# Kernel tuning notes

Hardware: AMD Instinct MI355X
Metric: run time of the kernel (lower is better)

## Reference

```python
import jax, jax.numpy as jnp
import numpy as np

NT, C, B, N, H, E = 32768, 128, 64, 512, 4, 524288  # total nodes, channels, graphs, nodes/graph, heads, edges
DH = C // H
EPS = 1e-5


def batchnorm(x, g, b):
    # BatchNorm1d over the node dimension (training-mode batch statistics)
    m = x.mean(axis=0)
    v = x.var(axis=0)
    return (x - m) * jax.lax.rsqrt(v + EPS) * g + b


def setup_inputs() -> dict:
    key = jax.random.key(0)
    ks = jax.random.split(key, 8)
    s = 1.0 / np.sqrt(C)
    return dict(
        x=jax.random.normal(ks[0], (NT, C), jnp.float32),
        edge_index=jax.random.randint(ks[1], (2, E), 0, NT, dtype=jnp.int32),
        Wc=jax.random.normal(ks[2], (C, C), jnp.float32) * s,
        bc=jnp.zeros((C,), jnp.float32),
        in_proj_w=jax.random.normal(ks[3], (3 * C, C), jnp.float32) * s,
        in_proj_b=jnp.zeros((3 * C,), jnp.float32),
        out_proj_w=jax.random.normal(ks[4], (C, C), jnp.float32) * s,
        out_proj_b=jnp.zeros((C,), jnp.float32),
        gn1=jnp.ones((C,), jnp.float32), bn1=jnp.zeros((C,), jnp.float32),
        gn2=jnp.ones((C,), jnp.float32), bn2=jnp.zeros((C,), jnp.float32),
        gn3=jnp.ones((C,), jnp.float32), bn3=jnp.zeros((C,), jnp.float32),
        Wm1=jax.random.normal(ks[5], (2 * C, C), jnp.float32) * s,
        bm1=jnp.zeros((2 * C,), jnp.float32),
        Wm2=jax.random.normal(ks[6], (C, 2 * C), jnp.float32) / np.sqrt(2 * C),
        bm2=jnp.zeros((C,), jnp.float32),
    )


def reference(x, edge_index, Wc, bc, in_proj_w, in_proj_b, out_proj_w, out_proj_b,
              gn1, bn1, gn2, bn2, gn3, bn3, Wm1, bm1, Wm2, bm2):
    # --- local branch: mean-aggregation message passing + linear + residual + BN ---
    src, dst = edge_index[0], edge_index[1]
    agg = jax.ops.segment_sum(x[src], dst, num_segments=NT)            # [NT, C]
    cnt = jax.ops.segment_sum(jnp.ones((E, 1), x.dtype), dst, num_segments=NT)
    agg = agg / jnp.maximum(cnt, 1.0)
    h_local = agg @ Wc.T + bc + x                                       # dropout p=0 -> no-op
    h_local = batchnorm(h_local, gn1, bn1)

    # --- global branch: to_dense_batch (equal-size graphs -> reshape) + MHA ---
    hd = x.reshape(B, N, C)
    qkv = hd @ in_proj_w.T + in_proj_b                                  # [B, N, 3C]
    q, k, v = jnp.split(qkv, 3, axis=-1)
    q = q.reshape(B, N, H, DH).transpose(0, 2, 1, 3)                    # [B, H, N, DH]
    k = k.reshape(B, N, H, DH).transpose(0, 2, 1, 3)
    v = v.reshape(B, N, H, DH).transpose(0, 2, 1, 3)
    scores = jnp.einsum('bhqd,bhkd->bhqk', q, k) / np.sqrt(DH)          # [B, H, N, N]
    attn = jax.nn.softmax(scores, axis=-1)
    o = jnp.einsum('bhqk,bhkd->bhqd', attn, v)                          # [B, H, N, DH]
    o = o.transpose(0, 2, 1, 3).reshape(B, N, C)
    h_attn = (o @ out_proj_w.T + out_proj_b).reshape(NT, C) + x
    h_attn = batchnorm(h_attn, gn2, bn2)

    # --- combine + MLP + final norm ---
    out = h_local + h_attn
    out = out + (jax.nn.relu(out @ Wm1.T + bm1) @ Wm2.T + bm2)
    return batchnorm(out, gn3, bn3)
```

## Files before the change

kernel.cpp:

```cpp
#include <hip/hip_runtime.h>
#include <cstddef>

#define NT    32768
#define CCH   128
#define BB    64
#define NNODE 512
#define NHEAD 4
#define DHEAD 32
#define EE    524288
#define EPS   1e-5f
#define MAXDEG 96

typedef unsigned short u16;
typedef unsigned int   u32;
typedef __attribute__((ext_vector_type(8))) short short8;
typedef __attribute__((ext_vector_type(4))) short short4v;
typedef __attribute__((ext_vector_type(4))) float f32x4;

__device__ __forceinline__ float b2f(u32 w) { return __uint_as_float(w << 16); }
__device__ __forceinline__ u16 f2b(float f) {
    u32 u = __float_as_uint(f);
    u += 0x7FFF + ((u >> 16) & 1);
    return (u16)(u >> 16);
}

__global__ __launch_bounds__(256) void prep_kernel(const float* __restrict__ x,
                                                   const float* __restrict__ Wc,
                                                   const float* __restrict__ Wqkv,
                                                   const float* __restrict__ Wo,
                                                   const float* __restrict__ Wm1,
                                                   const float* __restrict__ Wm2,
                                                   u16* __restrict__ xb,
                                                   u16* __restrict__ Wcb,
                                                   u16* __restrict__ Wqkvb,
                                                   u16* __restrict__ Wob,
                                                   u16* __restrict__ Wm1b,
                                                   u16* __restrict__ Wm2b,
                                                   const int* __restrict__ ei,
                                                   int* __restrict__ cursor,
                                                   int* __restrict__ bucket) {
    if (blockIdx.x >= 2120) {
        int e = (blockIdx.x - 2120) * 256 + threadIdx.x;
        int src = ei[e];
        int dst = ei[EE + e];
        int pos = atomicAdd(cursor + dst, 1);
        if (pos < MAXDEG) bucket[dst * MAXDEG + pos] = src;
        return;
    }
    int r = blockIdx.x * 256 + threadIdx.x;
    const float* src; u16* dst;
    if (r < 524288) { src = x; dst = xb; }
    else if ((r -= 524288) < 2048) { src = Wc; dst = Wcb; }
    else if ((r -= 2048) < 6144) { src = Wqkv; dst = Wqkvb; }
    else if ((r -= 6144) < 2048) { src = Wo; dst = Wob; }
    else if ((r -= 2048) < 4096) { src = Wm1; dst = Wm1b; }
    else { r -= 4096; src = Wm2; dst = Wm2b; }
    size_t base = (size_t)r * 8;
    float4 a = *(const float4*)(src + base);
    float4 b = *(const float4*)(src + base + 4);
    uint4 u;
    u.x = (u32)f2b(a.x) | ((u32)f2b(a.y) << 16);
    u.y = (u32)f2b(a.z) | ((u32)f2b(a.w) << 16);
    u.z = (u32)f2b(b.x) | ((u32)f2b(b.y) << 16);
    u.w = (u32)f2b(b.z) | ((u32)f2b(b.w) << 16);
    *(uint4*)(dst + base) = u;
}

__global__ __launch_bounds__(256) void aggregate(const int* __restrict__ bucket,
                                                 const int* __restrict__ cursor,
                                                 const u16* __restrict__ xb,
                                                 u16* __restrict__ agg) {
    int ln = threadIdx.x >> 5;
    int c4 = threadIdx.x & 31;
    int n = blockIdx.x * 8 + ln;
    __shared__ int srcs[8][MAXDEG];
    int d = min(cursor[n], MAXDEG);
    for (int j = c4; j < d; j += 32) srcs[ln][j] = bucket[n * MAXDEG + j];
    __syncthreads();
    float s0 = 0.f, s1 = 0.f, s2 = 0.f, s3 = 0.f;
    for (int j = 0; j < d; ++j) {
        uint2 w = *(const uint2*)(xb + (size_t)srcs[ln][j] * CCH + c4 * 4);
        s0 += b2f(w.x & 0xffffu);
        s1 += b2f(w.x >> 16);
        s2 += b2f(w.y & 0xffffu);
        s3 += b2f(w.y >> 16);
    }
    float inv = 1.0f / fmaxf((float)d, 1.0f);
    uint2 out;
    out.x = (u32)f2b(s0 * inv) | ((u32)f2b(s1 * inv) << 16);
    out.y = (u32)f2b(s2 * inv) | ((u32)f2b(s3 * inv) << 16);
    *(uint2*)(agg + (size_t)n * CCH + c4 * 4) = out;
}

template <bool RELU, int RESID, bool STATS>
__global__ __launch_bounds__(256) void gemm_mfma(const u16* __restrict__ A,
                                                 const u16* __restrict__ W,
                                                 const float* __restrict__ bias,
                                                 const u16* __restrict__ residb,
                                                 u16* __restrict__ outb,
                                                 float* __restrict__ sum,
                                                 float* __restrict__ sumsq,
                                                 int M, int N, int K) {
    __shared__ u16 As[128 * 32];
    __shared__ u16 Bs[128 * 32];
    __shared__ u16 Cs[4][16 * 72];
    __shared__ float csum[128];
    __shared__ float csq[128];
    int m0 = blockIdx.x * 128, n0 = blockIdx.y * 128;
    int tid = threadIdx.x;
    int lane = tid & 63, wave = tid >> 6;
    int wm = (wave & 1) * 64, wn = (wave >> 1) * 64;
    int l15 = lane & 15, l4 = lane >> 4;

    if (STATS) {
        if (tid < 128) { csum[tid] = 0.f; csq[tid] = 0.f; }
    }

    f32x4 zero = {0.f, 0.f, 0.f, 0.f};
    f32x4 acc[4][4];
#pragma unroll
    for (int i = 0; i < 4; ++i)
#pragma unroll
        for (int j = 0; j < 4; ++j) acc[i][j] = zero;

    int srow = tid >> 2;
    int scol = (tid & 3) * 8;

    int kIter = K >> 5;
    uint4 a0 = *(const uint4*)(A + (size_t)(m0 + srow) * K + scol);
    uint4 a1 = *(const uint4*)(A + (size_t)(m0 + srow + 64) * K + scol);
    uint4 b0 = *(const uint4*)(W + (size_t)(n0 + srow) * K + scol);
    uint4 b1 = *(const uint4*)(W + (size_t)(n0 + srow + 64) * K + scol);
    for (int ki = 0; ki < kIter; ++ki) {
        if (ki) __syncthreads();
        *(uint4*)&As[srow * 32 + scol] = a0;
        *(uint4*)&As[(srow + 64) * 32 + scol] = a1;
        *(uint4*)&Bs[srow * 32 + scol] = b0;
        *(uint4*)&Bs[(srow + 64) * 32 + scol] = b1;
        if (ki + 1 < kIter) {
            int k0 = (ki + 1) * 32;
            a0 = *(const uint4*)(A + (size_t)(m0 + srow) * K + k0 + scol);
            a1 = *(const uint4*)(A + (size_t)(m0 + srow + 64) * K + k0 + scol);
            b0 = *(const uint4*)(W + (size_t)(n0 + srow) * K + k0 + scol);
            b1 = *(const uint4*)(W + (size_t)(n0 + srow + 64) * K + k0 + scol);
        }
        __syncthreads();
        short8 af[4], bf[4];
#pragma unroll
        for (int t = 0; t < 4; ++t) {
            af[t] = *(const short8*)&As[(wm + t * 16 + l15) * 32 + l4 * 8];
            bf[t] = *(const short8*)&Bs[(wn + t * 16 + l15) * 32 + l4 * 8];
        }
#pragma unroll
        for (int mt = 0; mt < 4; ++mt)
#pragma unroll
            for (int nt = 0; nt < 4; ++nt)
                acc[mt][nt] = __builtin_amdgcn_mfma_f32_16x16x32_bf16(af[mt], bf[nt], acc[mt][nt], 0, 0, 0);
    }

    float ps[4] = {0.f, 0.f, 0.f, 0.f};
    float pq[4] = {0.f, 0.f, 0.f, 0.f};
    int rl = lane >> 3;
    int cg = lane & 7;
#pragma unroll
    for (int mt = 0; mt < 4; ++mt) {
#pragma unroll
        for (int nt = 0; nt < 4; ++nt) {
            int col = n0 + wn + nt * 16 + l15;
            float bs = bias[col];
#pragma unroll
            for (int r = 0; r < 4; ++r) {
                int row = m0 + wm + mt * 16 + l4 * 4 + r;
                float v = acc[mt][nt][r] + bs;
                if (RESID == 2) v += b2f(residb[(size_t)row * N + col]);
                if (RELU) v = fmaxf(v, 0.0f);
                Cs[wave][(l4 * 4 + r) * 72 + nt * 16 + l15] = f2b(v);
                if (STATS) { ps[nt] += v; pq[nt] += v * v; }
            }
        }
#pragma unroll
        for (int p = 0; p < 2; ++p) {
            int lrow = p * 8 + rl;
            uint4 wv = *(const uint4*)&Cs[wave][lrow * 72 + cg * 8];
            int grow = m0 + wm + mt * 16 + lrow;
            *(uint4*)(outb + (size_t)grow * N + n0 + wn + cg * 8) = wv;
        }
    }
    if (STATS) {
#pragma unroll
        for (int nt = 0; nt < 4; ++nt) {
            atomicAdd(&csum[wn + nt * 16 + l15], ps[nt]);
            atomicAdd(&csq[wn + nt * 16 + l15], pq[nt]);
        }
        __syncthreads();
        if (tid < 128) {
            atomicAdd(sum + n0 + tid, csum[tid]);
            atomicAdd(sumsq + n0 + tid, csq[tid]);
        }
    }
}

__global__ __launch_bounds__(256) void gemm_wc_qkv(const u16* __restrict__ aggb,
                                                   const u16* __restrict__ Wcb,
                                                   const float* __restrict__ bc,
                                                   const u16* __restrict__ xb,
                                                   u16* __restrict__ hlocb,
                                                   float* __restrict__ sum1,
                                                   float* __restrict__ sq1,
                                                   const u16* __restrict__ Wqkvb,
                                                   const float* __restrict__ bqkv,
                                                   u16* __restrict__ qkvb) {
    __shared__ u16 As[128 * 32];
    __shared__ u16 Bs[128 * 32];
    __shared__ u16 Cs[4][16 * 72];
    __shared__ float csum[128];
    __shared__ float csq[128];
    int y = blockIdx.y;
    bool wc = (y == 0);
    const u16* A = wc ? aggb : xb;
    const u16* W = wc ? Wcb : (Wqkvb + (size_t)(y - 1) * 128 * 128);
    const float* bias = wc ? bc : (bqkv + (y - 1) * 128);
    int ostride = wc ? 128 : 384;
    int ocol0 = wc ? 0 : (y - 1) * 128;
    u16* outp = wc ? hlocb : qkvb;

    int m0 = blockIdx.x * 128;
    int tid = threadIdx.x;
    int lane = tid & 63, wave = tid >> 6;
    int wm = (wave & 1) * 64, wn = (wave >> 1) * 64;
    int l15 = lane & 15, l4 = lane >> 4;

    if (wc && tid < 128) { csum[tid] = 0.f; csq[tid] = 0.f; }

    f32x4 zero = {0.f, 0.f, 0.f, 0.f};
    f32x4 acc[4][4];
#pragma unroll
    for (int i = 0; i < 4; ++i)
#pragma unroll
        for (int j = 0; j < 4; ++j) acc[i][j] = zero;

    int srow = tid >> 2;
    int scol = (tid & 3) * 8;

    uint4 a0 = *(const uint4*)(A + (size_t)(m0 + srow) * 128 + scol);
    uint4 a1 = *(const uint4*)(A + (size_t)(m0 + srow + 64) * 128 + scol);
    uint4 b0 = *(const uint4*)(W + (size_t)srow * 128 + scol);
    uint4 b1 = *(const uint4*)(W + (size_t)(srow + 64) * 128 + scol);
    for (int ki = 0; ki < 4; ++ki) {
        if (ki) __syncthreads();
        *(uint4*)&As[srow * 32 + scol] = a0;
        *(uint4*)&As[(srow + 64) * 32 + scol] = a1;
        *(uint4*)&Bs[srow * 32 + scol] = b0;
        *(uint4*)&Bs[(srow + 64) * 32 + scol] = b1;
        if (ki < 3) {
            int k0 = (ki + 1) * 32;
            a0 = *(const uint4*)(A + (size_t)(m0 + srow) * 128 + k0 + scol);
            a1 = *(const uint4*)(A + (size_t)(m0 + srow + 64) * 128 + k0 + scol);
            b0 = *(const uint4*)(W + (size_t)srow * 128 + k0 + scol);
            b1 = *(const uint4*)(W + (size_t)(srow + 64) * 128 + k0 + scol);
        }
        __syncthreads();
        short8 af[4], bf[4];
#pragma unroll
        for (int t = 0; t < 4; ++t) {
            af[t] = *(const short8*)&As[(wm + t * 16 + l15) * 32 + l4 * 8];
            bf[t] = *(const short8*)&Bs[(wn + t * 16 + l15) * 32 + l4 * 8];
        }
#pragma unroll
        for (int mt = 0; mt < 4; ++mt)
#pragma unroll
            for (int nt = 0; nt < 4; ++nt)
                acc[mt][nt] = __builtin_amdgcn_mfma_f32_16x16x32_bf16(af[mt], bf[nt], acc[mt][nt], 0, 0, 0);
    }

    float ps[4] = {0.f, 0.f, 0.f, 0.f};
    float pq[4] = {0.f, 0.f, 0.f, 0.f};
    int rl = lane >> 3;
    int cg = lane & 7;
#pragma unroll
    for (int mt = 0; mt < 4; ++mt) {
#pragma unroll
        for (int nt = 0; nt < 4; ++nt) {
            int lcol = wn + nt * 16 + l15;
            float bs = bias[lcol];
#pragma unroll
            for (int r = 0; r < 4; ++r) {
                int row = m0 + wm + mt * 16 + l4 * 4 + r;
                float v = acc[mt][nt][r] + bs;
                if (wc) v += b2f(xb[(size_t)row * 128 + lcol]);
                Cs[wave][(l4 * 4 + r) * 72 + nt * 16 + l15] = f2b(v);
                if (wc) { ps[nt] += v; pq[nt] += v * v; }
            }
        }
#pragma unroll
        for (int p = 0; p < 2; ++p) {
            int lrow = p * 8 + rl;
            uint4 wv = *(const uint4*)&Cs[wave][lrow * 72 + cg * 8];
            int grow = m0 + wm + mt * 16 + lrow;
            *(uint4*)(outp + (size_t)grow * ostride + ocol0 + wn + cg * 8) = wv;
        }
    }
    if (wc) {
#pragma unroll
        for (int nt = 0; nt < 4; ++nt) {
            atomicAdd(&csum[wn + nt * 16 + l15], ps[nt]);
            atomicAdd(&csq[wn + nt * 16 + l15], pq[nt]);
        }
        __syncthreads();
        if (tid < 128) {
            atomicAdd(sum1 + tid, csum[tid]);
            atomicAdd(sq1 + tid, csq[tid]);
        }
    }
}

__global__ __launch_bounds__(256) void gemm_m1c(const u16* __restrict__ hlocb,
                                                const u16* __restrict__ t2b,
                                                const float* __restrict__ sum1,
                                                const float* __restrict__ sq1,
                                                const float* __restrict__ g1,
                                                const float* __restrict__ bt1,
                                                const float* __restrict__ sum2,
                                                const float* __restrict__ sq2,
                                                const float* __restrict__ g2,
                                                const float* __restrict__ bt2,
                                                u16* __restrict__ shb,
                                                const u16* __restrict__ Wm1b,
                                                const float* __restrict__ bm1,
                                                u16* __restrict__ hidb) {
    __shared__ u16 As[128 * 32];
    __shared__ u16 Bs[128 * 32];
    __shared__ u16 Cs[4][16 * 72];
    __shared__ float AF1[128], BF1[128], AF2[128], BF2[128];
    int tid = threadIdx.x;
    {
        int c = tid & 127;
        const float* sm = (tid < 128) ? sum1 : sum2;
        const float* sq = (tid < 128) ? sq1 : sq2;
        const float* g  = (tid < 128) ? g1 : g2;
        const float* bt = (tid < 128) ? bt1 : bt2;
        float m = sm[c] * (1.0f / NT);
        float v = sq[c] * (1.0f / NT) - m * m;
        float a = g[c] * rsqrtf(v + EPS);
        if (tid < 128) { AF1[c] = a; BF1[c] = bt[c] - m * a; }
        else           { AF2[c] = a; BF2[c] = bt[c] - m * a; }
    }
    int m0 = blockIdx.x * 128, n0 = blockIdx.y * 128;
    int lane = tid & 63, wave = tid >> 6;
    int wm = (wave & 1) * 64, wn = (wave >> 1) * 64;
    int l15 = lane & 15, l4 = lane >> 4;

    f32x4 zero = {0.f, 0.f, 0.f, 0.f};
    f32x4 acc[4][4];
#pragma unroll
    for (int i = 0; i < 4; ++i)
#pragma unroll
        for (int j = 0; j < 4; ++j) acc[i][j] = zero;

    int srow = tid >> 2;
    int scol = (tid & 3) * 8;
    bool wr = (blockIdx.y == 0);

    uint4 h0 = *(const uint4*)(hlocb + (size_t)(m0 + srow) * 128 + scol);
    uint4 h1 = *(const uint4*)(hlocb + (size_t)(m0 + srow + 64) * 128 + scol);
    uint4 t0 = *(const uint4*)(t2b + (size_t)(m0 + srow) * 128 + scol);
    uint4 t1 = *(const uint4*)(t2b + (size_t)(m0 + srow + 64) * 128 + scol);
    uint4 b0 = *(const uint4*)(Wm1b + (size_t)(n0 + srow) * 128 + scol);
    uint4 b1 = *(const uint4*)(Wm1b + (size_t)(n0 + srow + 64) * 128 + scol);
    __syncthreads();
    for (int ki = 0; ki < 4; ++ki) {
        int k0 = ki * 32;
        if (ki) __syncthreads();
        uint4 c0, c1;
        {
            const u32 hw[4] = {h0.x, h0.y, h0.z, h0.w};
            const u32 tw[4] = {t0.x, t0.y, t0.z, t0.w};
            u32 ow[4];
#pragma unroll
            for (int p = 0; p < 4; ++p) {
                int cc = k0 + scol + p * 2;
                float v0 = AF1[cc] * b2f(hw[p] & 0xffffu) + BF1[cc] + AF2[cc] * b2f(tw[p] & 0xffffu) + BF2[cc];
                float v1 = AF1[cc + 1] * b2f(hw[p] >> 16) + BF1[cc + 1] + AF2[cc + 1] * b2f(tw[p] >> 16) + BF2[cc + 1];
                ow[p] = (u32)f2b(v0) | ((u32)f2b(v1) << 16);
            }
            c0.x = ow[0]; c0.y = ow[1]; c0.z = ow[2]; c0.w = ow[3];
        }
        {
            const u32 hw[4] = {h1.x, h1.y, h1.z, h1.w};
            const u32 tw[4] = {t1.x, t1.y, t1.z, t1.w};
            u32 ow[4];
#pragma unroll
            for (int p = 0; p < 4; ++p) {
                int cc = k0 + scol + p * 2;
                float v0 = AF1[cc] * b2f(hw[p] & 0xffffu) + BF1[cc] + AF2[cc] * b2f(tw[p] & 0xffffu) + BF2[cc];
                float v1 = AF1[cc + 1] * b2f(hw[p] >> 16) + BF1[cc + 1] + AF2[cc + 1] * b2f(tw[p] >> 16) + BF2[cc + 1];
                ow[p] = (u32)f2b(v0) | ((u32)f2b(v1) << 16);
            }
            c1.x = ow[0]; c1.y = ow[1]; c1.z = ow[2]; c1.w = ow[3];
        }
        *(uint4*)&As[srow * 32 + scol] = c0;
        *(uint4*)&As[(srow + 64) * 32 + scol] = c1;
        *(uint4*)&Bs[srow * 32 + scol] = b0;
        *(uint4*)&Bs[(srow + 64) * 32 + scol] = b1;
        if (wr) {
            *(uint4*)(shb + (size_t)(m0 + srow) * 128 + k0 + scol) = c0;
            *(uint4*)(shb + (size_t)(m0 + srow + 64) * 128 + k0 + scol) = c1;
        }
        if (ki < 3) {
            int kn = k0 + 32;
            h0 = *(const uint4*)(hlocb + (size_t)(m0 + srow) * 128 + kn + scol);
            h1 = *(const uint4*)(hlocb + (size_t)(m0 + srow + 64) * 128 + kn + scol);
            t0 = *(const uint4*)(t2b + (size_t)(m0 + srow) * 128 + kn + scol);
            t1 = *(const uint4*)(t2b + (size_t)(m0 + srow + 64) * 128 + kn + scol);
            b0 = *(const uint4*)(Wm1b + (size_t)(n0 + srow) * 128 + kn + scol);
            b1 = *(const uint4*)(Wm1b + (size_t)(n0 + srow + 64) * 128 + kn + scol);
        }
        __syncthreads();
        short8 af[4], bf[4];
#pragma unroll
        for (int t = 0; t < 4; ++t) {
            af[t] = *(const short8*)&As[(wm + t * 16 + l15) * 32 + l4 * 8];
            bf[t] = *(const short8*)&Bs[(wn + t * 16 + l15) * 32 + l4 * 8];
        }
#pragma unroll
        for (int mt = 0; mt < 4; ++mt)
#pragma unroll
            for (int nt = 0; nt < 4; ++nt)
                acc[mt][nt] = __builtin_amdgcn_mfma_f32_16x16x32_bf16(af[mt], bf[nt], acc[mt][nt], 0, 0, 0);
    }

    int rl = lane >> 3;
    int cg = lane & 7;
#pragma unroll
    for (int mt = 0; mt < 4; ++mt) {
#pragma unroll
        for (int nt = 0; nt < 4; ++nt) {
            int col = n0 + wn + nt * 16 + l15;
            float bs = bm1[col];
#pragma unroll
            for (int r = 0; r < 4; ++r) {
                float v = fmaxf(acc[mt][nt][r] + bs, 0.0f);
                Cs[wave][(l4 * 4 + r) * 72 + nt * 16 + l15] = f2b(v);
            }
        }
#pragma unroll
        for (int p = 0; p < 2; ++p) {
            int lrow = p * 8 + rl;
            uint4 wv = *(const uint4*)&Cs[wave][lrow * 72 + cg * 8];
            int grow = m0 + wm + mt * 16 + lrow;
            *(uint4*)(hidb + (size_t)grow * 256 + n0 + wn + cg * 8) = wv;
        }
    }
}

__global__ __launch_bounds__(256) void final_bn(const u16* __restrict__ X,
                                                const float* __restrict__ sum3,
                                                const float* __restrict__ sq3,
                                                const float* __restrict__ g3,
                                                const float* __restrict__ bt3,
                                                float* __restrict__ outp) {
    __shared__ float A3[128], B3[128];
    int t = threadIdx.x;
    if (t < 128) {
        float m = sum3[t] * (1.0f / NT);
        float v = sq3[t] * (1.0f / NT) - m * m;
        float a = g3[t] * rsqrtf(v + EPS);
        A3[t] = a;
        B3[t] = bt3[t] - m * a;
    }
    __syncthreads();
    int i8 = blockIdx.x * 256 + t;
    size_t i = (size_t)i8 * 8;
    int c = (int)(i & (CCH - 1));
    uint4 u = *(const uint4*)(X + i);
    float x[8];
    x[0] = b2f(u.x & 0xffffu); x[1] = b2f(u.x >> 16);
    x[2] = b2f(u.y & 0xffffu); x[3] = b2f(u.y >> 16);
    x[4] = b2f(u.z & 0xffffu); x[5] = b2f(u.z >> 16);
    x[6] = b2f(u.w & 0xffffu); x[7] = b2f(u.w >> 16);
    float4 o0, o1;
    o0.x = A3[c + 0] * x[0] + B3[c + 0];
    o0.y = A3[c + 1] * x[1] + B3[c + 1];
    o0.z = A3[c + 2] * x[2] + B3[c + 2];
    o0.w = A3[c + 3] * x[3] + B3[c + 3];
    o1.x = A3[c + 4] * x[4] + B3[c + 4];
    o1.y = A3[c + 5] * x[5] + B3[c + 5];
    o1.z = A3[c + 6] * x[6] + B3[c + 6];
    o1.w = A3[c + 7] * x[7] + B3[c + 7];
    *(float4*)(outp + i) = o0;
    *(float4*)(outp + i + 4) = o1;
}

__global__ __launch_bounds__(512) void attn_mfma(const u16* __restrict__ qkv,
                                                 u16* __restrict__ o) {
    __shared__ __align__(16) u16 Ks[512 * 40];
    __shared__ __align__(16) u16 Vt[32 * 520];
    int bh = blockIdx.x;
    int b = bh >> 2, h = bh & 3;
    int tid = threadIdx.x;
    int lane = tid & 63, wave = tid >> 6;
    int quad = lane >> 4, l15 = lane & 15;
    const float scale = 0.1767766952966369f;

    const u16* kvbase = qkv + (size_t)b * 512 * 384 + 128 + h * 32;
    for (int idx = tid; idx < 2048; idx += 512) {
        int row = idx >> 2, c = idx & 3;
        *(uint4*)&Ks[row * 40 + c * 8] = *(const uint4*)(kvbase + (size_t)row * 384 + c * 8);
    }
    for (int idx = tid; idx < 2048; idx += 512) {
        int row = idx >> 2, c = idx & 3;
        uint4 u = *(const uint4*)(kvbase + 128 + (size_t)row * 384 + c * 8);
        u16 e[8];
        *(uint4*)e = u;
#pragma unroll
        for (int i = 0; i < 8; ++i) Vt[(c * 8 + i) * 520 + row] = e[i];
    }
    __syncthreads();

    f32x4 zero = {0.f, 0.f, 0.f, 0.f};
    for (int qt = 0; qt < 4; ++qt) {
        int qbase = wave * 64 + qt * 16;
        short8 qf = *(const short8*)(qkv + (size_t)(b * 512 + qbase + l15) * 384 + h * 32 + quad * 8);
        float lq = 0.f;
        f32x4 oa[2] = {zero, zero};

        for (int kv0 = 0; kv0 < 512; kv0 += 64) {
            f32x4 s[4];
#pragma unroll
            for (int t = 0; t < 4; ++t) {
                short8 kb = *(const short8*)&Ks[(kv0 + t * 16 + l15) * 40 + quad * 8];
                s[t] = __builtin_amdgcn_mfma_f32_16x16x32_bf16(kb, qf, zero, 0, 0, 0);
            }
            short8 pa[4];
#pragma unroll
            for (int t = 0; t < 4; ++t) {
                float p0 = __expf(s[t][0] * scale);
                float p1 = __expf(s[t][1] * scale);
                float p2 = __expf(s[t][2] * scale);
                float p3 = __expf(s[t][3] * scale);
                lq += (p0 + p1) + (p2 + p3);
                short8 a8 = {(short)f2b(p0), (short)f2b(p1), (short)f2b(p2), (short)f2b(p3), 0, 0, 0, 0};
                pa[t] = a8;
            }
#pragma unroll
            for (int t = 0; t < 4; ++t) {
                int tbase = kv0 + t * 16;
#pragma unroll
                for (int n = 0; n < 2; ++n) {
                    short4v v4 = *(const short4v*)&Vt[(n * 16 + l15) * 520 + tbase + quad * 4];
                    short8 vb = {v4.x, v4.y, v4.z, v4.w, 0, 0, 0, 0};
                    oa[n] = __builtin_amdgcn_mfma_f32_16x16x32_bf16(pa[t], vb, oa[n], 0, 0, 0);
                }
            }
        }
        lq += __shfl_xor(lq, 16);
        lq += __shfl_xor(lq, 32);
        u16* op = o + (size_t)(b * 512 + qbase) * 128 + h * 32;
#pragma unroll
        for (int r = 0; r < 4; ++r) {
            float Lr = __shfl(lq, quad * 4 + r);
            float inv = 1.0f / Lr;
#pragma unroll
            for (int n = 0; n < 2; ++n)
                op[(quad * 4 + r) * 128 + n * 16 + l15] = f2b(oa[n][r] * inv);
        }
    }
}

extern "C" void kernel_launch(void* const* d_in, const int* in_sizes, int n_in,
                              void* d_out, int out_size, void* d_ws, size_t ws_size,
                              hipStream_t stream) {
    const float* x    = (const float*)d_in[0];
    const int*   ei   = (const int*)d_in[1];
    const float* Wc   = (const float*)d_in[2];
    const float* bc   = (const float*)d_in[3];
    const float* Wqkv = (const float*)d_in[4];
    const float* bqkv = (const float*)d_in[5];
    const float* Wo   = (const float*)d_in[6];
    const float* bo   = (const float*)d_in[7];
    const float* gn1  = (const float*)d_in[8];
    const float* bn1b = (const float*)d_in[9];
    const float* gn2  = (const float*)d_in[10];
    const float* bn2b = (const float*)d_in[11];
    const float* gn3  = (const float*)d_in[12];
    const float* bn3b = (const float*)d_in[13];
    const float* Wm1  = (const float*)d_in[14];
    const float* bm1  = (const float*)d_in[15];
    const float* Wm2  = (const float*)d_in[16];
    const float* bm2  = (const float*)d_in[17];
    float* outp = (float*)d_out;

    char* w = (char*)d_ws;
    const size_t MB = 1024 * 1024;
    u16* xb    = (u16*)(w);
    u16* hlocb = (u16*)(w + 8 * MB);
    u16* t2b   = (u16*)(w + 16 * MB);
    u16* out2b = (u16*)(w + 24 * MB);
    u16* qkvb  = (u16*)(w + 32 * MB);
    u16* hidb  = (u16*)(w + 56 * MB);
    u16* shb   = (u16*)(w + 72 * MB);
    int* bucket = (int*)(w + 80 * MB);
    int* cursor = (int*)(w + 92 * MB);
    float* stats = (float*)(w + 92 * MB + 128 * 1024);
    u16* Wcb   = (u16*)(w + 93 * MB);
    u16* Wqkvb = Wcb + 16384;
    u16* Wob   = Wqkvb + 49152;
    u16* Wm1b  = Wob + 16384;
    u16* Wm2b  = Wm1b + 32768;
    float* sum1 = stats;        float* sq1 = stats + 128;
    float* sum2 = stats + 256;  float* sq2 = stats + 384;
    float* sum3 = stats + 512;  float* sq3 = stats + 640;

    hipMemsetAsync(cursor, 0, 128 * 1024 + 6 * 128 * 4, stream);

    prep_kernel<<<2120 + 2048, 256, 0, stream>>>(x, Wc, Wqkv, Wo, Wm1, Wm2,
                                                 xb, Wcb, Wqkvb, Wob, Wm1b, Wm2b,
                                                 ei, cursor, bucket);

    aggregate<<<NT / 8, 256, 0, stream>>>(bucket, cursor, xb, shb);

    {
        dim3 g(NT / 128, 4);
        gemm_wc_qkv<<<g, 256, 0, stream>>>(shb, Wcb, bc, xb, hlocb, sum1, sq1,
                                           Wqkvb, bqkv, qkvb);
    }

    attn_mfma<<<BB * NHEAD, 512, 0, stream>>>(qkvb, shb);

    {
        dim3 g(NT / 128, 1);
        gemm_mfma<false, 2, true><<<g, 256, 0, stream>>>(
            shb, Wob, bo, xb, t2b, sum2, sq2, NT, 128, 128);
    }

    {
        dim3 g(NT / 128, 2);
        gemm_m1c<<<g, 256, 0, stream>>>(hlocb, t2b, sum1, sq1, gn1, bn1b,
                                        sum2, sq2, gn2, bn2b, shb, Wm1b, bm1, hidb);
    }

    {
        dim3 g(NT / 128, 1);
        gemm_mfma<false, 2, true><<<g, 256, 0, stream>>>(
            hidb, Wm2b, bm2, shb, out2b, sum3, sq3, NT, 128, 256);
    }

    final_bn<<<NT * CCH / 8 / 256, 256, 0, stream>>>(out2b, sum3, sq3, gn3, bn3b, outp);
}
```

Measured before the change: 249.0 us.

## Merge aggregation with QKV projection into one launch, move Wc GEMM after attention

Combines the neighbor-mean aggregation and the QKV projection GEMM into a single heterogeneous launch, with the first 4096 blocks doing aggregation and the rest doing QKV tiles, so the two independent jobs can run at the same time. The Wc projection with residual and BN1 statistics is split out into a separate gemm_mfma launch after attention, and attention now writes to its own buffer. This drops one dependency step before attention but adds a kernel launch and a re-read of the aggregated buffer.

```diff
diff --git a/kernel.cpp b/kernel.cpp
--- a/kernel.cpp
+++ b/kernel.cpp
@@ -66,30 +66,188 @@
     *(uint4*)(dst + base) = u;
 }
 
-__global__ __launch_bounds__(256) void aggregate(const int* __restrict__ bucket,
-                                                 const int* __restrict__ cursor,
-                                                 const u16* __restrict__ xb,
-                                                 u16* __restrict__ agg) {
-    int ln = threadIdx.x >> 5;
-    int c4 = threadIdx.x & 31;
-    int n = blockIdx.x * 8 + ln;
-    __shared__ int srcs[8][MAXDEG];
-    int d = min(cursor[n], MAXDEG);
-    for (int j = c4; j < d; j += 32) srcs[ln][j] = bucket[n * MAXDEG + j];
+__global__ __launch_bounds__(256) void stage2_kernel(const int* __restrict__ bucket,
+                                                     const int* __restrict__ cursor,
+                                                     const u16* __restrict__ xb,
+                                                     u16* __restrict__ aggb,
+                                                     const u16* __restrict__ Wqkvb,
+                                                     const float* __restrict__ bqkv,
+                                                     u16* __restrict__ qkvb) {
+    __shared__ __align__(16) char smem[26624];
+    int tid = threadIdx.x;
+    if (blockIdx.x < 4096) {
+        int* srcs = (int*)smem;
+        int ln = tid >> 5;
+        int c4 = tid & 31;
+        int n = blockIdx.x * 8 + ln;
+        int d = min(cursor[n], MAXDEG);
+        for (int j = c4; j < d; j += 32) srcs[ln * MAXDEG + j] = bucket[n * MAXDEG + j];
+        __syncthreads();
+        float s0 = 0.f, s1 = 0.f, s2 = 0.f, s3 = 0.f;
+        for (int j = 0; j < d; ++j) {
+            uint2 w = *(const uint2*)(xb + (size_t)srcs[ln * MAXDEG + j] * CCH + c4 * 4);
+            s0 += b2f(w.x & 0xffffu);
+            s1 += b2f(w.x >> 16);
+            s2 += b2f(w.y & 0xffffu);
+            s3 += b2f(w.y >> 16);
+        }
+        float inv = 1.0f / fmaxf((float)d, 1.0f);
+        uint2 out;
+        out.x = (u32)f2b(s0 * inv) | ((u32)f2b(s1 * inv) << 16);
+        out.y = (u32)f2b(s2 * inv) | ((u32)f2b(s3 * inv) << 16);
+        *(uint2*)(aggb + (size_t)n * CCH + c4 * 4) = out;
+        return;
+    }
+    int bx = blockIdx.x - 4096;
+    int y = bx >> 8;
+    int m0 = (bx & 255) * 128;
+    const u16* W = Wqkvb + (size_t)y * 128 * 128;
+    const float* bias = bqkv + y * 128;
+    u16* As = (u16*)smem;
+    u16* Bs = (u16*)(smem + 8192);
+    u16* Cs = (u16*)(smem + 16384);
+
+    int lane = tid & 63, wave = tid >> 6;
+    int wm = (wave & 1) * 64, wn = (wave >> 1) * 64;
+    int l15 = lane & 15, l4 = lane >> 4;
+
+    f32x4 zero = {0.f, 0.f, 0.f, 0.f};
+    f32x4 acc[4][4];
+#pragma unroll
+    for (int i = 0; i < 4; ++i)
+#pragma unroll
+        for (int j = 0; j < 4; ++j) acc[i][j] = zero;
+
+    int srow = tid >> 2;
+    int scol = (tid & 3) * 8;
+
+    uint4 a0 = *(const uint4*)(xb + (size_t)(m0 + srow) * 128 + scol);
+    uint4 a1 = *(const uint4*)(xb + (size_t)(m0 + srow + 64) * 128 + scol);
+    uint4 b0 = *(const uint4*)(W + (size_t)srow * 128 + scol);
+    uint4 b1 = *(const uint4*)(W + (size_t)(srow + 64) * 128 + scol);
+    for (int ki = 0; ki < 4; ++ki) {
+        if (ki) __syncthreads();
+        *(uint4*)&As[srow * 32 + scol] = a0;
+        *(uint4*)&As[(srow + 64) * 32 + scol] = a1;
+        *(uint4*)&Bs[srow * 32 + scol] = b0;
+        *(uint4*)&Bs[(srow + 64) * 32 + scol] = b1;
+        if (ki < 3) {
+            int k0 = (ki + 1) * 32;
+            a0 = *(const uint4*)(xb + (size_t)(m0 + srow) * 128 + k0 + scol);
+            a1 = *(const uint4*)(xb + (size_t)(m0 + srow + 64) * 128 + k0 + scol);
+            b0 = *(const uint4*)(W + (size_t)srow * 128 + k0 + scol);
+            b1 = *(const uint4*)(W + (size_t)(srow + 64) * 128 + k0 + scol);
+        }
+        __syncthreads();
+        short8 af[4], bf[4];
+#pragma unroll
+        for (int t = 0; t < 4; ++t) {
+            af[t] = *(const short8*)&As[(wm + t * 16 + l15) * 32 + l4 * 8];
+            bf[t] = *(const short8*)&Bs[(wn + t * 16 + l15) * 32 + l4 * 8];
+        }
+#pragma unroll
+        for (int mt = 0; mt < 4; ++mt)
+#pragma unroll
+            for (int nt = 0; nt < 4; ++nt)
+                acc[mt][nt] = __builtin_amdgcn_mfma_f32_16x16x32_bf16(af[mt], bf[nt], acc[mt][nt], 0, 0, 0);
+    }
+
+    int rl = lane >> 3;
+    int cg = lane & 7;
+    u16* Cw = Cs + wave * 16 * 72;
+#pragma unroll
+    for (int mt = 0; mt < 4; ++mt) {
+#pragma unroll
+        for (int nt = 0; nt < 4; ++nt) {
+            float bs = bias[wn + nt * 16 + l15];
+#pragma unroll
+            for (int r = 0; r < 4; ++r)
+                Cw[(l4 * 4 + r) * 72 + nt * 16 + l15] = f2b(acc[mt][nt][r] + bs);
+        }
+#pragma unroll
+        for (int p = 0; p < 2; ++p) {
+            int lrow = p * 8 + rl;
+            uint4 wv = *(const uint4*)&Cw[lrow * 72 + cg * 8];
+            int grow = m0 + wm + mt * 16 + lrow;
+            *(uint4*)(qkvb + (size_t)grow * 384 + y * 128 + wn + cg * 8) = wv;
+        }
+    }
+}
+
+__global__ __launch_bounds__(512) void attn_mfma(const u16* __restrict__ qkv,
+                                                 u16* __restrict__ o) {
+    __shared__ __align__(16) u16 Ks[512 * 40];
+    __shared__ __align__(16) u16 Vt[32 * 520];
+    int bh = blockIdx.x;
+    int b = bh >> 2, h = bh & 3;
+    int tid = threadIdx.x;
+    int lane = tid & 63, wave = tid >> 6;
+    int quad = lane >> 4, l15 = lane & 15;
+    const float scale = 0.1767766952966369f;
+
+    const u16* kvbase = qkv + (size_t)b * 512 * 384 + 128 + h * 32;
+    for (int idx = tid; idx < 2048; idx += 512) {
+        int row = idx >> 2, c = idx & 3;
+        *(uint4*)&Ks[row * 40 + c * 8] = *(const uint4*)(kvbase + (size_t)row * 384 + c * 8);
+    }
+    for (int idx = tid; idx < 2048; idx += 512) {
+        int row = idx >> 2, c = idx & 3;
+        uint4 u = *(const uint4*)(kvbase + 128 + (size_t)row * 384 + c * 8);
+        u16 e[8];
+        *(uint4*)e = u;
+#pragma unroll
+        for (int i = 0; i < 8; ++i) Vt[(c * 8 + i) * 520 + row] = e[i];
+    }
     __syncthreads();
-    float s0 = 0.f, s1 = 0.f, s2 = 0.f, s3 = 0.f;
-    for (int j = 0; j < d; ++j) {
-        uint2 w = *(const uint2*)(xb + (size_t)srcs[ln][j] * CCH + c4 * 4);
-        s0 += b2f(w.x & 0xffffu);
-        s1 += b2f(w.x >> 16);
-        s2 += b2f(w.y & 0xffffu);
-        s3 += b2f(w.y >> 16);
-    }
-    float inv = 1.0f / fmaxf((float)d, 1.0f);
-    uint2 out;
-    out.x = (u32)f2b(s0 * inv) | ((u32)f2b(s1 * inv) << 16);
-    out.y = (u32)f2b(s2 * inv) | ((u32)f2b(s3 * inv) << 16);
-    *(uint2*)(agg + (size_t)n * CCH + c4 * 4) = out;
+
+    f32x4 zero = {0.f, 0.f, 0.f, 0.f};
+    for (int qt = 0; qt < 4; ++qt) {
+        int qbase = wave * 64 + qt * 16;
+        short8 qf = *(const short8*)(qkv + (size_t)(b * 512 + qbase + l15) * 384 + h * 32 + quad * 8);
+        float lq = 0.f;
+        f32x4 oa[2] = {zero, zero};
+
+        for (int kv0 = 0; kv0 < 512; kv0 += 64) {
+            f32x4 s[4];
+#pragma unroll
+            for (int t = 0; t < 4; ++t) {
+                short8 kb = *(const short8*)&Ks[(kv0 + t * 16 + l15) * 40 + quad * 8];
+                s[t] = __builtin_amdgcn_mfma_f32_16x16x32_bf16(kb, qf, zero, 0, 0, 0);
+            }
+            short8 pa[4];
+#pragma unroll
+            for (int t = 0; t < 4; ++t) {
+                float p0 = __expf(s[t][0] * scale);
+                float p1 = __expf(s[t][1] * scale);
+                float p2 = __expf(s[t][2] * scale);
+                float p3 = __expf(s[t][3] * scale);
+                lq += (p0 + p1) + (p2 + p3);
+                short8 a8 = {(short)f2b(p0), (short)f2b(p1), (short)f2b(p2), (short)f2b(p3), 0, 0, 0, 0};
+                pa[t] = a8;
+            }
+#pragma unroll
+            for (int t = 0; t < 4; ++t) {
+                int tbase = kv0 + t * 16;
+#pragma unroll
+                for (int n = 0; n < 2; ++n) {
+                    short4v v4 = *(const short4v*)&Vt[(n * 16 + l15) * 520 + tbase + quad * 4];
+                    short8 vb = {v4.x, v4.y, v4.z, v4.w, 0, 0, 0, 0};
+                    oa[n] = __builtin_amdgcn_mfma_f32_16x16x32_bf16(pa[t], vb, oa[n], 0, 0, 0);
+                }
+            }
+        }
+        lq += __shfl_xor(lq, 16);
+        lq += __shfl_xor(lq, 32);
+        u16* op = o + (size_t)(b * 512 + qbase) * 128 + h * 32;
+#pragma unroll
+        for (int r = 0; r < 4; ++r) {
+            float Lr = __shfl(lq, quad * 4 + r);
+            float inv = 1.0f / Lr;
+#pragma unroll
+            for (int n = 0; n < 2; ++n)
+                op[(quad * 4 + r) * 128 + n * 16 + l15] = f2b(oa[n][r] * inv);
+        }
+    }
 }
 
 template <bool RELU, int RESID, bool STATS>
@@ -196,120 +354,6 @@
         if (tid < 128) {
             atomicAdd(sum + n0 + tid, csum[tid]);
             atomicAdd(sumsq + n0 + tid, csq[tid]);
-        }
-    }
-}
-
-__global__ __launch_bounds__(256) void gemm_wc_qkv(const u16* __restrict__ aggb,
-                                                   const u16* __restrict__ Wcb,
-                                                   const float* __restrict__ bc,
-                                                   const u16* __restrict__ xb,
-                                                   u16* __restrict__ hlocb,
-                                                   float* __restrict__ sum1,
-                                                   float* __restrict__ sq1,
-                                                   const u16* __restrict__ Wqkvb,
-                                                   const float* __restrict__ bqkv,
-                                                   u16* __restrict__ qkvb) {
-    __shared__ u16 As[128 * 32];
-    __shared__ u16 Bs[128 * 32];
-    __shared__ u16 Cs[4][16 * 72];
-    __shared__ float csum[128];
-    __shared__ float csq[128];
-    int y = blockIdx.y;
-    bool wc = (y == 0);
-    const u16* A = wc ? aggb : xb;
-    const u16* W = wc ? Wcb : (Wqkvb + (size_t)(y - 1) * 128 * 128);
-    const float* bias = wc ? bc : (bqkv + (y - 1) * 128);
-    int ostride = wc ? 128 : 384;
-    int ocol0 = wc ? 0 : (y - 1) * 128;
-    u16* outp = wc ? hlocb : qkvb;
-
-    int m0 = blockIdx.x * 128;
-    int tid = threadIdx.x;
-    int lane = tid & 63, wave = tid >> 6;
-    int wm = (wave & 1) * 64, wn = (wave >> 1) * 64;
-    int l15 = lane & 15, l4 = lane >> 4;
-
-    if (wc && tid < 128) { csum[tid] = 0.f; csq[tid] = 0.f; }
-
-    f32x4 zero = {0.f, 0.f, 0.f, 0.f};
-    f32x4 acc[4][4];
-#pragma unroll
-    for (int i = 0; i < 4; ++i)
-#pragma unroll
-        for (int j = 0; j < 4; ++j) acc[i][j] = zero;
-
-    int srow = tid >> 2;
-    int scol = (tid & 3) * 8;
-
-    uint4 a0 = *(const uint4*)(A + (size_t)(m0 + srow) * 128 + scol);
-    uint4 a1 = *(const uint4*)(A + (size_t)(m0 + srow + 64) * 128 + scol);
-    uint4 b0 = *(const uint4*)(W + (size_t)srow * 128 + scol);
-    uint4 b1 = *(const uint4*)(W + (size_t)(srow + 64) * 128 + scol);
-    for (int ki = 0; ki < 4; ++ki) {
-        if (ki) __syncthreads();
-        *(uint4*)&As[srow * 32 + scol] = a0;
-        *(uint4*)&As[(srow + 64) * 32 + scol] = a1;
-        *(uint4*)&Bs[srow * 32 + scol] = b0;
-        *(uint4*)&Bs[(srow + 64) * 32 + scol] = b1;
-        if (ki < 3) {
-            int k0 = (ki + 1) * 32;
-            a0 = *(const uint4*)(A + (size_t)(m0 + srow) * 128 + k0 + scol);
-            a1 = *(const uint4*)(A + (size_t)(m0 + srow + 64) * 128 + k0 + scol);
-            b0 = *(const uint4*)(W + (size_t)srow * 128 + k0 + scol);
-            b1 = *(const uint4*)(W + (size_t)(srow + 64) * 128 + k0 + scol);
-        }
-        __syncthreads();
-        short8 af[4], bf[4];
-#pragma unroll
-        for (int t = 0; t < 4; ++t) {
-            af[t] = *(const short8*)&As[(wm + t * 16 + l15) * 32 + l4 * 8];
-            bf[t] = *(const short8*)&Bs[(wn + t * 16 + l15) * 32 + l4 * 8];
-        }
-#pragma unroll
-        for (int mt = 0; mt < 4; ++mt)
-#pragma unroll
-            for (int nt = 0; nt < 4; ++nt)
-                acc[mt][nt] = __builtin_amdgcn_mfma_f32_16x16x32_bf16(af[mt], bf[nt], acc[mt][nt], 0, 0, 0);
-    }
-
-    float ps[4] = {0.f, 0.f, 0.f, 0.f};
-    float pq[4] = {0.f, 0.f, 0.f, 0.f};
-    int rl = lane >> 3;
-    int cg = lane & 7;
-#pragma unroll
-    for (int mt = 0; mt < 4; ++mt) {
-#pragma unroll
-        for (int nt = 0; nt < 4; ++nt) {
-            int lcol = wn + nt * 16 + l15;
-            float bs = bias[lcol];
-#pragma unroll
-            for (int r = 0; r < 4; ++r) {
-                int row = m0 + wm + mt * 16 + l4 * 4 + r;
-                float v = acc[mt][nt][r] + bs;
-                if (wc) v += b2f(xb[(size_t)row * 128 + lcol]);
-                Cs[wave][(l4 * 4 + r) * 72 + nt * 16 + l15] = f2b(v);
-                if (wc) { ps[nt] += v; pq[nt] += v * v; }
-            }
-        }
-#pragma unroll
-        for (int p = 0; p < 2; ++p) {
-            int lrow = p * 8 + rl;
-            uint4 wv = *(const uint4*)&Cs[wave][lrow * 72 + cg * 8];
-            int grow = m0 + wm + mt * 16 + lrow;
-            *(uint4*)(outp + (size_t)grow * ostride + ocol0 + wn + cg * 8) = wv;
-        }
-    }
-    if (wc) {
-#pragma unroll
-        for (int nt = 0; nt < 4; ++nt) {
-            atomicAdd(&csum[wn + nt * 16 + l15], ps[nt]);
-            atomicAdd(&csq[wn + nt * 16 + l15], pq[nt]);
-        }
-        __syncthreads();
-        if (tid < 128) {
-            atomicAdd(sum1 + tid, csum[tid]);
-            atomicAdd(sq1 + tid, csq[tid]);
         }
     }
 }
@@ -491,82 +535,6 @@
     *(float4*)(outp + i + 4) = o1;
 }
 
-__global__ __launch_bounds__(512) void attn_mfma(const u16* __restrict__ qkv,
-                                                 u16* __restrict__ o) {
-    __shared__ __align__(16) u16 Ks[512 * 40];
-    __shared__ __align__(16) u16 Vt[32 * 520];
-    int bh = blockIdx.x;
-    int b = bh >> 2, h = bh & 3;
-    int tid = threadIdx.x;
-    int lane = tid & 63, wave = tid >> 6;
-    int quad = lane >> 4, l15 = lane & 15;
-    const float scale = 0.1767766952966369f;
-
-    const u16* kvbase = qkv + (size_t)b * 512 * 384 + 128 + h * 32;
-    for (int idx = tid; idx < 2048; idx += 512) {
-        int row = idx >> 2, c = idx & 3;
-        *(uint4*)&Ks[row * 40 + c * 8] = *(const uint4*)(kvbase + (size_t)row * 384 + c * 8);
-    }
-    for (int idx = tid; idx < 2048; idx += 512) {
-        int row = idx >> 2, c = idx & 3;
-        uint4 u = *(const uint4*)(kvbase + 128 + (size_t)row * 384 + c * 8);
-        u16 e[8];
-        *(uint4*)e = u;
-#pragma unroll
-        for (int i = 0; i < 8; ++i) Vt[(c * 8 + i) * 520 + row] = e[i];
-    }
-    __syncthreads();
-
-    f32x4 zero = {0.f, 0.f, 0.f, 0.f};
-    for (int qt = 0; qt < 4; ++qt) {
-        int qbase = wave * 64 + qt * 16;
-        short8 qf = *(const short8*)(qkv + (size_t)(b * 512 + qbase + l15) * 384 + h * 32 + quad * 8);
-        float lq = 0.f;
-        f32x4 oa[2] = {zero, zero};
-
-        for (int kv0 = 0; kv0 < 512; kv0 += 64) {
-            f32x4 s[4];
-#pragma unroll
-            for (int t = 0; t < 4; ++t) {
-                short8 kb = *(const short8*)&Ks[(kv0 + t * 16 + l15) * 40 + quad * 8];
-                s[t] = __builtin_amdgcn_mfma_f32_16x16x32_bf16(kb, qf, zero, 0, 0, 0);
-            }
-            short8 pa[4];
-#pragma unroll
-            for (int t = 0; t < 4; ++t) {
-                float p0 = __expf(s[t][0] * scale);
-                float p1 = __expf(s[t][1] * scale);
-                float p2 = __expf(s[t][2] * scale);
-                float p3 = __expf(s[t][3] * scale);
-                lq += (p0 + p1) + (p2 + p3);
-                short8 a8 = {(short)f2b(p0), (short)f2b(p1), (short)f2b(p2), (short)f2b(p3), 0, 0, 0, 0};
-                pa[t] = a8;
-            }
-#pragma unroll
-            for (int t = 0; t < 4; ++t) {
-                int tbase = kv0 + t * 16;
-#pragma unroll
-                for (int n = 0; n < 2; ++n) {
-                    short4v v4 = *(const short4v*)&Vt[(n * 16 + l15) * 520 + tbase + quad * 4];
-                    short8 vb = {v4.x, v4.y, v4.z, v4.w, 0, 0, 0, 0};
-                    oa[n] = __builtin_amdgcn_mfma_f32_16x16x32_bf16(pa[t], vb, oa[n], 0, 0, 0);
-                }
-            }
-        }
-        lq += __shfl_xor(lq, 16);
-        lq += __shfl_xor(lq, 32);
-        u16* op = o + (size_t)(b * 512 + qbase) * 128 + h * 32;
-#pragma unroll
-        for (int r = 0; r < 4; ++r) {
-            float Lr = __shfl(lq, quad * 4 + r);
-            float inv = 1.0f / Lr;
-#pragma unroll
-            for (int n = 0; n < 2; ++n)
-                op[(quad * 4 + r) * 128 + n * 16 + l15] = f2b(oa[n][r] * inv);
-        }
-    }
-}
-
 extern "C" void kernel_launch(void* const* d_in, const int* in_sizes, int n_in,
                               void* d_out, int out_size, void* d_ws, size_t ws_size,
                               hipStream_t stream) {
@@ -607,6 +575,7 @@
     u16* Wob   = Wqkvb + 49152;
     u16* Wm1b  = Wob + 16384;
     u16* Wm2b  = Wm1b + 32768;
+    u16* ob    = (u16*)(w + 94 * MB);
     float* sum1 = stats;        float* sq1 = stats + 128;
     float* sum2 = stats + 256;  float* sq2 = stats + 384;
     float* sum3 = stats + 512;  float* sq3 = stats + 640;
@@ -617,20 +586,21 @@
                                                  xb, Wcb, Wqkvb, Wob, Wm1b, Wm2b,
                                                  ei, cursor, bucket);
 
-    aggregate<<<NT / 8, 256, 0, stream>>>(bucket, cursor, xb, shb);
-
-    {
-        dim3 g(NT / 128, 4);
-        gemm_wc_qkv<<<g, 256, 0, stream>>>(shb, Wcb, bc, xb, hlocb, sum1, sq1,
-                                           Wqkvb, bqkv, qkvb);
-    }
-
-    attn_mfma<<<BB * NHEAD, 512, 0, stream>>>(qkvb, shb);
+    stage2_kernel<<<4096 + 768, 256, 0, stream>>>(bucket, cursor, xb, shb,
+                                                  Wqkvb, bqkv, qkvb);
+
+    attn_mfma<<<BB * NHEAD, 512, 0, stream>>>(qkvb, ob);
 
     {
         dim3 g(NT / 128, 1);
         gemm_mfma<false, 2, true><<<g, 256, 0, stream>>>(
-            shb, Wob, bo, xb, t2b, sum2, sq2, NT, 128, 128);
+            shb, Wcb, bc, xb, hlocb, sum1, sq1, NT, 128, 128);
+    }
+
+    {
+        dim3 g(NT / 128, 1);
+        gemm_mfma<false, 2, true><<<g, 256, 0, stream>>>(
+            ob, Wob, bo, xb, t2b, sum2, sq2, NT, 128, 128);
     }
 
     {
```

After: 257.3 us. 3.3% more time.
